# Performance work log

Hardware: AMD Instinct MI355X
Metric: run time of the kernel (lower is better)

## Reference

```python
import jax, jax.numpy as jnp
import numpy as np
from jax import lax

EPS = 1e-5

def _conv(x, w, pad):
    return lax.conv_general_dilated(x, w, (1, 1), [(pad, pad), (pad, pad)],
                                    dimension_numbers=('NCHW', 'OIHW', 'NCHW'))

def _bn(x, g, b, m, v):
    inv = g * jax.lax.rsqrt(v + EPS)
    return x * inv[None, :, None, None] + (b - m * inv)[None, :, None, None]

def _deform(x, ow, ob):
    # ConvOffset2d: 3x3 conv predicts 2*C per-channel (dy,dx) offsets, then
    # bilinear resample each channel at (grid + offset), clipped to the image.
    B, C, H, W = x.shape
    off = _conv(x, ow, 1) + ob[None, :, None, None]          # [B,2C,H,W]
    off = off.reshape(B, C, 2, H, W)
    yy = jnp.arange(H, dtype=x.dtype)[:, None]
    xx = jnp.arange(W, dtype=x.dtype)[None, :]
    py = jnp.clip(yy + off[:, :, 0], 0.0, H - 1)             # [B,C,H,W]
    px = jnp.clip(xx + off[:, :, 1], 0.0, W - 1)
    y0 = jnp.floor(py).astype(jnp.int32)
    x0 = jnp.floor(px).astype(jnp.int32)
    y1 = jnp.minimum(y0 + 1, H - 1)
    x1 = jnp.minimum(x0 + 1, W - 1)
    wy = py - y0.astype(x.dtype)
    wx = px - x0.astype(x.dtype)
    flat = x.reshape(B, C, H * W)
    def g(yi, xi):
        idx = (yi * W + xi).reshape(B, C, H * W)
        return jnp.take_along_axis(flat, idx, axis=2).reshape(B, C, H, W)
    v00, v01, v10, v11 = g(y0, x0), g(y0, x1), g(y1, x0), g(y1, x1)
    return (v00 * (1 - wy) * (1 - wx) + v01 * (1 - wy) * wx +
            v10 * wy * (1 - wx) + v11 * wy * wx)

def setup_inputs() -> dict:
    key = jax.random.key(0)
    ks = jax.random.split(key, 32)
    B, Cin, Cmid, H, W = 4, 1024, 256, 64, 64
    d = {}
    d['x'] = jax.random.normal(ks[0], (B, Cin, H, W), jnp.float32)
    # offset-predicting convs (3x3, C -> 2C), small init so offsets ~O(1)
    d['ow1'] = jax.random.normal(ks[1], (2 * Cin, Cin, 3, 3), jnp.float32) * 0.01
    d['ob1'] = jnp.zeros((2 * Cin,), jnp.float32)
    d['ow2'] = jax.random.normal(ks[2], (2 * Cmid, Cmid, 3, 3), jnp.float32) * 0.01
    d['ob2'] = jnp.zeros((2 * Cmid,), jnp.float32)
    d['ow3'] = jax.random.normal(ks[3], (2 * Cmid, Cmid, 3, 3), jnp.float32) * 0.01
    d['ob3'] = jnp.zeros((2 * Cmid,), jnp.float32)
    # bottleneck convs (no bias, as in ResNet)
    d['w1'] = jax.random.normal(ks[4], (Cmid, Cin, 1, 1), jnp.float32) * (1.0 / np.sqrt(Cin))
    d['w2'] = jax.random.normal(ks[5], (Cmid, Cmid, 3, 3), jnp.float32) * (1.0 / np.sqrt(9 * Cmid))
    d['w3'] = jax.random.normal(ks[6], (Cin, Cmid, 1, 1), jnp.float32) * (1.0 / np.sqrt(Cmid))
    # batchnorm (inference) params
    for i, c in zip((1, 2, 3), (Cmid, Cmid, Cin)):
        d[f'g{i}'] = jnp.ones((c,), jnp.float32)
        d[f'b{i}'] = jnp.zeros((c,), jnp.float32)
        d[f'm{i}'] = jax.random.normal(ks[10 + i], (c,), jnp.float32) * 0.1
        d[f'v{i}'] = jnp.ones((c,), jnp.float32) + jax.random.uniform(ks[20 + i], (c,), jnp.float32) * 0.1
    return d

def reference(x, ow1, ob1, w1, g1, b1, m1, v1,
              ow2, ob2, w2, g2, b2, m2, v2,
              ow3, ob3, w3, g3, b3, m3, v3):
    h = _deform(x, ow1, ob1)
    h = _bn(_conv(h, w1, 0), g1, b1, m1, v1)
    h = _deform(h, ow2, ob2)
    h = _bn(_conv(h, w2, 1), g2, b2, m2, v2)
    h = _deform(h, ow3, ob3)
    h = _bn(_conv(h, w3, 0), g3, b3, m3, v3)
    return jax.nn.relu(h)
```

## Files before the change

kernel.cpp:

```cpp
#include <hip/hip_runtime.h>


typedef unsigned short u16;
typedef __bf16 bf16x8 __attribute__((ext_vector_type(8)));
typedef float f32x4 __attribute__((ext_vector_type(4)));
typedef _Float16 f16;

__device__ __forceinline__ u16 f2bf(float f) {
  unsigned u = __float_as_uint(f);
  u += 0x7fffu + ((u >> 16) & 1u);
  return (u16)(u >> 16);
}
__device__ __forceinline__ float bf2f(u16 h) { return __uint_as_float((unsigned)h << 16); }
__device__ __forceinline__ u16 f2h(float f) { f16 h = (f16)f; return __builtin_bit_cast(u16, h); }
__device__ __forceinline__ float h2f(u16 u) { return (float)__builtin_bit_cast(f16, u); }

__device__ __forceinline__ void gload16(const u16* g, u16* l) {
  __builtin_amdgcn_global_load_lds((__attribute__((address_space(1))) unsigned int*)g,
                                   (__attribute__((address_space(3))) unsigned int*)l,
                                   16, 0, 0);
}

#define VM8() asm volatile("s_waitcnt vmcnt(8)" ::: "memory")
#define VM4() asm volatile("s_waitcnt vmcnt(4)" ::: "memory")
#define VM0() asm volatile("s_waitcnt vmcnt(0)" ::: "memory")
#define BAR()                                   \
  do {                                          \
    asm volatile("" ::: "memory");              \
    __builtin_amdgcn_s_barrier();               \
    asm volatile("" ::: "memory");              \
  } while (0)
#define LGK0()                                          \
  do {                                                  \
    asm volatile("s_waitcnt lgkmcnt(0)" ::: "memory");  \
    __builtin_amdgcn_sched_barrier(0);                  \
  } while (0)

__global__ __launch_bounds__(256) void zero_k(uint4* __restrict__ p, unsigned n) {
  unsigned i = blockIdx.x * 256u + threadIdx.x;
  const unsigned st = gridDim.x * 256u;
  uint4 z; z.x = 0u; z.y = 0u; z.z = 0u; z.w = 0u;
  for (; i < n; i += st) p[i] = z;
}

template <int SPLIT>
__global__ __launch_bounds__(256) void pack_w(const float* __restrict__ w,
                                              u16* __restrict__ hi, u16* __restrict__ lo,
                                              int M, int C, int T) {
  const int AK = C * T;
  const int id = blockIdx.x * 256 + threadIdx.x;
  if (id >= M * AK) return;
  const int j = id & 7;
  const int slot = (id >> 3) & 511;
  const int rest = id >> 12;
  const int steps = AK >> 5;
  const int step = rest % steps;
  const int mt = rest / steps;
  const int kg = slot >> 7, m = slot & 127;
  const int k = step * 32 + kg * 8 + j;
  const int tap = k / C;
  const int c = k - tap * C;
  const int mg = mt * 128 + m;
  const float v = w[((size_t)mg * C + c) * T + tap];
  const u16 h = f2bf(v);
  hi[id] = h;
  if (SPLIT) lo[id] = f2bf(v - bf2f(h));
}

template <int CC, int T>
__global__ __launch_bounds__(256) void pack8_w(const float* __restrict__ w,
                                               u16* __restrict__ dst, int M) {
  constexpr int KT2 = 2 * (T * CC / 64);
  const int id = blockIdx.x * 256 + threadIdx.x;
  if (id >= M * CC * T) return;
  const int j = id & 7;
  const int d = (id >> 3) & 1023;
  const int rest = id >> 13;
  const int H = rest % KT2;
  const int mt = rest / KT2;
  const int row = d >> 2, kq = d & 3;
  const int k = H * 32 + ((kq ^ ((row >> 1) & 3)) * 8) + j;
  const int tap = k / CC, c = k - tap * CC;
  const int oc = mt * 256 + row;
  dst[id] = f2bf(w[((size_t)oc * CC + c) * T + tap]);
}

__global__ __launch_bounds__(256) void prep_x(const float* __restrict__ x,
                                              u16* __restrict__ xp) {
  __shared__ float t[64][65];
  const int c0 = blockIdx.x * 64;
  const int y = blockIdx.y;
  const int b = blockIdx.z;
  const int tid = threadIdx.x;
#pragma unroll
  for (int i = 0; i < 16; ++i) {
    const int idx = i * 256 + tid;
    const int ci = idx >> 6, xi = idx & 63;
    t[ci][xi] = x[(((size_t)b * 1024 + c0 + ci) * 64 + y) * 64 + xi];
  }
  __syncthreads();
#pragma unroll
  for (int i = 0; i < 16; ++i) {
    const int idx = i * 256 + tid;
    const int xi = idx >> 6, ci = idx & 63;
    xp[((size_t)((b * 66 + y + 1) * 66 + (xi + 1))) * 1024 + c0 + ci] = f2bf(t[ci][xi]);
  }
}

template <int C, int PADDST>
__global__ __launch_bounds__(256) void deform_k(const u16* __restrict__ src,
                                                const u16* __restrict__ off,
                                                u16* __restrict__ dst) {
  const int id = blockIdx.x * 256 + threadIdx.x;
  const int c = id & (C - 1);
  const int pix = id / C;
  const int b = pix >> 12;
  const int y = (pix >> 6) & 63;
  const int x = pix & 63;
  const unsigned ov = *(const unsigned*)(off + (size_t)pix * (2 * C) + 2 * c);
  const float py = fminf(fmaxf((float)y + h2f((u16)(ov & 0xffffu)), 0.f), 63.f);
  const float px = fminf(fmaxf((float)x + h2f((u16)(ov >> 16)), 0.f), 63.f);
  const int y0i = (int)py, x0i = (int)px;
  const int y1i = min(y0i + 1, 63), x1i = min(x0i + 1, 63);
  const float wy = py - (float)y0i, wx = px - (float)x0i;
  const int bb66 = b * 66;
  auto at = [&](int yi, int xi) -> size_t {
    return ((size_t)((bb66 + yi + 1) * 66 + (xi + 1))) * C + c;
  };
  const float v00 = bf2f(src[at(y0i, x0i)]);
  const float v01 = bf2f(src[at(y0i, x1i)]);
  const float v10 = bf2f(src[at(y1i, x0i)]);
  const float v11 = bf2f(src[at(y1i, x1i)]);
  const float val = v00 * (1.f - wy) * (1.f - wx) + v01 * (1.f - wy) * wx +
                    v10 * wy * (1.f - wx) + v11 * wy * wx;
  const size_t d = PADDST ? at(y, x) : (size_t)id;
  dst[d] = f2bf(val);
}

template <int TAPS, int CC, int NMT>
__global__ __launch_bounds__(512, 2) void gemm8_conv(
    const u16* __restrict__ Apack, const u16* __restrict__ Bsrc,
    const float* __restrict__ bias, u16* __restrict__ out, int M) {
  constexpr int KT = TAPS * CC / 64;
  constexpr int KT2 = 2 * KT;
  __shared__ u16 lds[65536];
  const int tid = threadIdx.x;
  const int w = tid >> 6, lane = tid & 63;
  const int wm = w >> 2, wn = w & 3;
  const int kg = lane >> 4, lm = lane & 15;
  const int g = blockIdx.x;
  const int local = g >> 3;
  const int mt = local % NMT;
  const int nt = (g & 7) * 8 + local / NMT;
  const int b_img = nt >> 4;
  const int y0 = (nt & 15) * 4;
  const u16* Abase = Apack + (size_t)mt * KT2 * 8192;

  f32x4 acc[8][4];
  const f32x4 fz = {0.f, 0.f, 0.f, 0.f};
#pragma unroll
  for (int i = 0; i < 8; ++i)
#pragma unroll
    for (int j = 0; j < 4; ++j) acc[i][j] = fz;

  auto rbase = [&](int b, int op, int kh) -> unsigned {
    return (unsigned)(((b * 2 + op) * 2 + kh) * 8192);
  };
  auto stage = [&](int H, int op) {
    if (H >= KT2) return;
    const unsigned dstb = rbase((H >> 1) & 1, op, H & 1);
#pragma unroll
    for (int it = 0; it < 2; ++it) {
      const int d = it * 512 + tid;
      u16* ldst = (u16*)&lds[dstb + (unsigned)(it * 512 + (tid & ~63)) * 8];
      if (op == 0) {
        gload16(Abase + (size_t)H * 8192 + (size_t)d * 8, ldst);
      } else {
        const int pl = d >> 2, kq = d & 3;
        const int kglob = H * 32;
        const int tap = (TAPS == 1) ? 0 : (kglob / CC);
        const int cbase = kglob - tap * CC;
        const int ky = (TAPS == 9) ? tap / 3 : 0, kx = (TAPS == 9) ? tap % 3 : 0;
        const int r = pl >> 6, xc = pl & 63;
        const size_t gb = ((size_t)((b_img * 66 + y0 + r + ky) * 66 + (xc + kx))) * CC +
                          (size_t)(cbase + ((kq ^ ((pl >> 1) & 3)) * 8));
        gload16(Bsrc + gb, ldst);
      }
    }
  };

#define PHASE(MG_, KH_, STH_, STOP_, WAIT_)                                          \
  {                                                                                  \
    const unsigned regA = rbase(bi, 0, KH_);                                         \
    if (MG_ == 0) {                                                                  \
      const unsigned regB = rbase(bi, 1, KH_);                                       \
      _Pragma("unroll") for (int nf = 0; nf < 4; ++nf) {                             \
        const int pc = wn * 64 + nf * 16 + lm;                                       \
        bfrag[nf] = *(const bf16x8*)&lds[regB + pc * 32 + (kg ^ ((pc >> 1) & 3)) * 8]; \
      }                                                                              \
    }                                                                                \
    bf16x8 afrag[4];                                                                 \
    _Pragma("unroll") for (int f = 0; f < 4; ++f) {                                  \
      const int row = wm * 128 + (MG_ * 4 + f) * 16 + lm;                            \
      afrag[f] = *(const bf16x8*)&lds[regA + row * 32 + (kg ^ ((row >> 1) & 3)) * 8];  \
    }                                                                                \
    stage(STH_, STOP_);                                                              \
    BAR();                                                                           \
    LGK0();                                                                          \
    __builtin_amdgcn_s_setprio(1);                                                   \
    _Pragma("unroll") for (int f = 0; f < 4; ++f)                                    \
        _Pragma("unroll") for (int nf = 0; nf < 4; ++nf)                             \
            acc[MG_ * 4 + f][nf] = __builtin_amdgcn_mfma_f32_16x16x32_bf16(          \
                afrag[f], bfrag[nf], acc[MG_ * 4 + f][nf], 0, 0, 0);                 \
    __builtin_amdgcn_s_setprio(0);                                                   \
    WAIT_;                                                                           \
    BAR();                                                                           \
  }

  stage(0, 0); stage(0, 1);
  stage(1, 0); stage(1, 1);
  stage(2, 0); stage(2, 1);
  VM8();
  BAR();

  for (int t = 0; t < KT; ++t) {
    const int bi = t & 1;
    bf16x8 bfrag[4];
    PHASE(0, 0, 2 * t + 3, 0, (void)0);
    PHASE(1, 0, 2 * t + 3, 1, do { if (t == KT - 1) VM0(); else VM8(); } while (0));
    PHASE(0, 1, 2 * t + 4, 0, (void)0);
    PHASE(1, 1, 2 * t + 4, 1,
          do { if (t == KT - 2) VM4(); else if (t < KT - 2) VM8(); } while (0));
  }
#undef PHASE

  const int ocb = mt * 256 + wm * 128 + kg * 4;
#pragma unroll
  for (int mf = 0; mf < 8; ++mf) {
    const int oc0 = ocb + mf * 16;
    const f32x4 bv = *(const f32x4*)&bias[oc0];
#pragma unroll
    for (int nf = 0; nf < 4; ++nf) {
      const int pix = nt * 256 + wn * 64 + nf * 16 + lm;
      f32x4 r = acc[mf][nf] + bv;
      uint2 hv;
      hv.x = (unsigned)f2h(r[0]) | ((unsigned)f2h(r[1]) << 16);
      hv.y = (unsigned)f2h(r[2]) | ((unsigned)f2h(r[3]) << 16);
      *(uint2*)(out + (size_t)pix * M + oc0) = hv;
    }
  }
}

template <int TAPS, int PAD, int EPI, int CC, int WSPLIT>
__global__ __launch_bounds__(256, 2) void gemm_conv(
    const u16* __restrict__ Aph, const u16* __restrict__ Apl,
    const u16* __restrict__ Bh,
    const float* __restrict__ p0, const float* __restrict__ p1,
    const float* __restrict__ p2, const float* __restrict__ p3,
    float* __restrict__ outF, u16* __restrict__ o16a, int M) {
  constexpr int NB = 2 + WSPLIT;
  __shared__ u16 lds[NB * 4096];
  constexpr int steps = TAPS * (CC / 32);
  const int tid = threadIdx.x;
  const int w = tid >> 6, lane = tid & 63;
  const int wm = (w >> 1) * 64, wn = (w & 1) * 64;
  const int kg = lane >> 4, lm = lane & 15;
  const int wg = blockIdx.x;
  const int chunk = (int)(gridDim.x >> 3);
  const int g = (wg & 7) * chunk + (wg >> 3);
  const int mt = g >> 7, nt = g & 127;
  const int b_img = nt >> 5;
  const int y0 = (nt & 31) * 2;

  f32x4 acc[4][4];
  const f32x4 fz = {0.f, 0.f, 0.f, 0.f};
#pragma unroll
  for (int i = 0; i < 4; ++i)
#pragma unroll
    for (int j = 0; j < 4; ++j) acc[i][j] = fz;

  const u16* Abase_h = Aph + (size_t)mt * steps * 4096;
  const u16* Abase_l = WSPLIT ? (Apl + (size_t)mt * steps * 4096) : nullptr;

  for (int step = 0; step < steps; ++step) {
    const int tap = (TAPS == 1) ? 0 : (step / (CC / 32));
    const int c0 = (step - tap * (CC / 32)) * 32;
    const int ky = (TAPS == 9) ? (tap / 3) : 0;
    const int kx = (TAPS == 9) ? (tap % 3) : 0;

#pragma unroll
    for (int it = 0; it < 2; ++it) {
      const int slot = w * 128 + it * 64 + lane;
      const unsigned ldso = (unsigned)(w * 128 + it * 64) * 8u;
      const size_t ga = (size_t)step * 4096 + (size_t)slot * 8;
      gload16(Abase_h + ga, &lds[0 * 4096 + ldso]);
      if (WSPLIT) gload16(Abase_l + ga, &lds[1 * 4096 + ldso]);
      const int n = slot >> 2, kq = slot & 3;
      const int kga = kq ^ ((n >> 1) & 3);
      size_t gb;
      if (PAD) {
        const int r = n >> 6, xc = n & 63;
        gb = ((size_t)((b_img * 66 + (y0 + r + ky)) * 66 + (xc + kx))) * CC +
             (size_t)(c0 + kga * 8);
      } else {
        gb = (size_t)(nt * 128 + n) * CC + (size_t)(c0 + kga * 8);
      }
      gload16(Bh + gb, &lds[(NB - 1) * 4096 + ldso]);
    }
    __syncthreads();

    bf16x8 ah[4], al[4], bh[4];
#pragma unroll
    for (int f = 0; f < 4; ++f) {
      const unsigned ao = (unsigned)(kg * 128 + wm + f * 16 + lm) * 8u;
      ah[f] = *(const bf16x8*)&lds[0 * 4096 + ao];
      if (WSPLIT) al[f] = *(const bf16x8*)&lds[1 * 4096 + ao];
      const int n = wn + f * 16 + lm;
      const unsigned bo = (unsigned)(n * 4 + (kg ^ ((n >> 1) & 3))) * 8u;
      bh[f] = *(const bf16x8*)&lds[(NB - 1) * 4096 + bo];
    }
#pragma unroll
    for (int i = 0; i < 4; ++i)
#pragma unroll
      for (int j = 0; j < 4; ++j) {
        acc[i][j] = __builtin_amdgcn_mfma_f32_16x16x32_bf16(ah[i], bh[j], acc[i][j], 0, 0, 0);
        if (WSPLIT)
          acc[i][j] = __builtin_amdgcn_mfma_f32_16x16x32_bf16(al[i], bh[j], acc[i][j], 0, 0, 0);
      }
    __syncthreads();
  }

  const int ocb = mt * 128 + wm + kg * 4;
#pragma unroll
  for (int fi = 0; fi < 4; ++fi) {
    const int oc0 = ocb + fi * 16;
    f32x4 scl, sft;
    if (EPI == 0) {
#pragma unroll
      for (int j = 0; j < 4; ++j) { scl[j] = 1.f; sft[j] = p0[oc0 + j]; }
    } else {
#pragma unroll
      for (int j = 0; j < 4; ++j) {
        const float inv = p0[oc0 + j] / sqrtf(p3[oc0 + j] + 1e-5f);
        scl[j] = inv;
        sft[j] = p1[oc0 + j] - p2[oc0 + j] * inv;
      }
    }
#pragma unroll
    for (int fj = 0; fj < 4; ++fj) {
      const int pix = nt * 128 + wn + fj * 16 + lm;
      f32x4 r = acc[fi][fj] * scl + sft;
      if (EPI == 0) {
        uint2 hv;
        hv.x = (unsigned)f2h(r[0]) | ((unsigned)f2h(r[1]) << 16);
        hv.y = (unsigned)f2h(r[2]) | ((unsigned)f2h(r[3]) << 16);
        *(uint2*)(o16a + (size_t)pix * M + oc0) = hv;
      } else if (EPI == 1) {
        const int bb = pix >> 12, yy = (pix >> 6) & 63, xx = pix & 63;
        const size_t pp = ((size_t)((bb * 66 + yy + 1) * 66 + (xx + 1))) * M + oc0;
        uint2 hv;
        hv.x = (unsigned)f2bf(r[0]) | ((unsigned)f2bf(r[1]) << 16);
        hv.y = (unsigned)f2bf(r[2]) | ((unsigned)f2bf(r[3]) << 16);
        *(uint2*)(o16a + pp) = hv;
      } else {
        const int bb = pix >> 12, pin = pix & 4095;
#pragma unroll
        for (int j = 0; j < 4; ++j)
          outF[((size_t)(bb * M + oc0 + j)) * 4096 + pin] = fmaxf(r[j], 0.f);
      }
    }
  }
}

extern "C" void kernel_launch(void* const* d_in, const int* in_sizes, int n_in,
                              void* d_out, int out_size, void* d_ws, size_t ws_size,
                              hipStream_t stream) {
  (void)in_sizes; (void)out_size;
  if (n_in < 22) return;
  const float* x   = (const float*)d_in[0];
  const float* ow1 = (const float*)d_in[1];
  const float* ob1 = (const float*)d_in[2];
  const float* ow2 = (const float*)d_in[3];
  const float* ob2 = (const float*)d_in[4];
  const float* ow3 = (const float*)d_in[5];
  const float* ob3 = (const float*)d_in[6];
  const float* w1  = (const float*)d_in[7];
  const float* w2  = (const float*)d_in[8];
  const float* w3  = (const float*)d_in[9];
  const float* g1 = (const float*)d_in[10], *b1 = (const float*)d_in[11];
  const float* m1 = (const float*)d_in[12], *v1 = (const float*)d_in[13];
  const float* g2 = (const float*)d_in[14], *b2 = (const float*)d_in[15];
  const float* m2 = (const float*)d_in[16], *v2 = (const float*)d_in[17];
  const float* g3 = (const float*)d_in[18], *b3 = (const float*)d_in[19];
  const float* m3 = (const float*)d_in[20], *v3 = (const float*)d_in[21];

  char* W = (char*)d_ws;
  constexpr size_t P66_1024 = 4ull * 66 * 66 * 1024 * 2;
  constexpr size_t P66_256  = 4ull * 66 * 66 * 256 * 2;
  constexpr size_t SZ_OFF1  = 4ull * 4096 * 2048 * 2;
  constexpr size_t SZ_OFF2  = 4ull * 4096 * 512 * 2;
  constexpr size_t SZ_H1    = 4ull * 4096 * 1024 * 2;
  constexpr size_t SZ_H3    = 4ull * 4096 * 256 * 2;
  constexpr size_t SZ_OW1 = 2048ull * 9216 * 2;
  constexpr size_t SZ_W1  = 256ull * 1024 * 2;
  constexpr size_t SZ_OW2 = 512ull * 2304 * 2;
  constexpr size_t SZ_W2  = 256ull * 2304 * 2;
  constexpr size_t SZ_OW3 = 512ull * 2304 * 2;
  constexpr size_t SZ_W3  = 1024ull * 256 * 2;

  constexpr size_t o_ow1h = 0;
  constexpr size_t o_xp   = o_ow1h + SZ_OW1;
  constexpr size_t o_off1 = o_xp + P66_1024;
  constexpr size_t o_t1p  = o_off1;
  constexpr size_t o_off2 = o_t1p + P66_256;
  constexpr size_t o_h2p  = o_off2 + SZ_OFF2;
  constexpr size_t o_t2p  = o_h2p + P66_256;
  static_assert(o_t2p + P66_256 <= o_off1 + SZ_OFF1, "era2 fits off1 slot");
  constexpr size_t o_h1   = o_off1 + SZ_OFF1;
  constexpr size_t o_off3 = o_h1;
  constexpr size_t o_h3   = o_off3 + SZ_OFF2;
  static_assert(o_h3 + SZ_H3 <= o_h1 + SZ_H1, "off3+h3 fit h1 slot");
  constexpr size_t o_w1h  = o_h1 + SZ_H1;
  constexpr size_t o_w1l  = o_w1h + SZ_W1;
  constexpr size_t o_ow2h = o_w1l + SZ_W1;
  constexpr size_t o_w2h  = o_ow2h + SZ_OW2;
  constexpr size_t o_w2l  = o_w2h + SZ_W2;
  constexpr size_t o_ow3h = o_w2l + SZ_W2;
  constexpr size_t o_w3h  = o_ow3h + SZ_OW3;
  constexpr size_t o_w3l  = o_w3h + SZ_W3;
  constexpr size_t WS_NEED = o_w3l + SZ_W3;
  if (ws_size < WS_NEED) return;

  auto U = [&](size_t o) { return (u16*)(W + o); };
  auto zero = [&](size_t off, size_t bytes) {
    const unsigned n = (unsigned)(bytes / 16);
    unsigned grid = (n + 255) / 256; if (grid > 4096) grid = 4096;
    zero_k<<<grid, 256, 0, stream>>>((uint4*)(W + off), n);
  };

  {
    int n;
    n = 2048 * 9216; pack8_w<1024, 9><<<(n + 255) / 256, 256, 0, stream>>>(ow1, U(o_ow1h), 2048);
    n = 512 * 2304;  pack8_w<256, 9><<<(n + 255) / 256, 256, 0, stream>>>(ow2, U(o_ow2h), 512);
    n = 512 * 2304;  pack8_w<256, 9><<<(n + 255) / 256, 256, 0, stream>>>(ow3, U(o_ow3h), 512);
    n = 256 * 1024;  pack_w<1><<<(n + 255) / 256, 256, 0, stream>>>(w1, U(o_w1h), U(o_w1l), 256, 1024, 1);
    n = 256 * 2304;  pack_w<1><<<(n + 255) / 256, 256, 0, stream>>>(w2, U(o_w2h), U(o_w2l), 256, 256, 9);
    n = 1024 * 256;  pack_w<1><<<(n + 255) / 256, 256, 0, stream>>>(w3, U(o_w3h), U(o_w3l), 1024, 256, 1);
  }

  zero(o_xp, P66_1024);
  prep_x<<<dim3(16, 64, 4), 256, 0, stream>>>(x, U(o_xp));

  gemm8_conv<9, 1024, 8><<<512, 512, 0, stream>>>(
      U(o_ow1h), U(o_xp), ob1, U(o_off1), 2048);
  deform_k<1024, 0><<<65536, 256, 0, stream>>>(U(o_xp), U(o_off1), U(o_h1));

  zero(o_t1p, P66_256);
  zero(o_h2p, 2 * P66_256);
  gemm_conv<1, 0, 1, 1024, 1><<<256, 256, 0, stream>>>(
      U(o_w1h), U(o_w1l), U(o_h1), g1, b1, m1, v1, nullptr, U(o_t1p), 256);
  gemm8_conv<9, 256, 2><<<128, 512, 0, stream>>>(
      U(o_ow2h), U(o_t1p), ob2, U(o_off2), 512);
  deform_k<256, 1><<<16384, 256, 0, stream>>>(U(o_t1p), U(o_off2), U(o_h2p));
  gemm_conv<9, 1, 1, 256, 1><<<256, 256, 0, stream>>>(
      U(o_w2h), U(o_w2l), U(o_h2p), g2, b2, m2, v2, nullptr, U(o_t2p), 256);
  gemm8_conv<9, 256, 2><<<128, 512, 0, stream>>>(
      U(o_ow3h), U(o_t2p), ob3, U(o_off3), 512);
  deform_k<256, 0><<<16384, 256, 0, stream>>>(U(o_t2p), U(o_off3), U(o_h3));
  gemm_conv<1, 0, 2, 256, 1><<<1024, 256, 0, stream>>>(
      U(o_w3h), U(o_w3l), U(o_h3), g3, b3, m3, v3, (float*)d_out, nullptr, 1024);
}
```

Before: 1.128 ms.

## Software-pipeline LDS fragment reads in gemm8 and drop split-bf16 weight precision

Restructures the big offset-conv GEMM main loop so LDS fragment reads for the next MFMA group are issued before the current group's MFMAs, with per-lane global addresses precomputed once and A/B staging split into separate issue points. Separately switches all bottleneck and small offset convs from hi/lo split-bf16 weights to single bf16 (SPLIT=0), removing the lo workspace and halving MFMA work there. The small offset convs also move from gemm8_conv to gemm_conv. Precision drop risks accuracy, and the reordered waitcnt schedule risks hazards.

```diff
diff --git a/kernel.cpp b/kernel.cpp
--- a/kernel.cpp
+++ b/kernel.cpp
@@ -22,7 +22,7 @@
 }
 
 #define VM8() asm volatile("s_waitcnt vmcnt(8)" ::: "memory")
-#define VM4() asm volatile("s_waitcnt vmcnt(4)" ::: "memory")
+#define VM6() asm volatile("s_waitcnt vmcnt(6)" ::: "memory")
 #define VM0() asm volatile("s_waitcnt vmcnt(0)" ::: "memory")
 #define BAR()                                   \
   do {                                          \
@@ -35,6 +35,7 @@
     asm volatile("s_waitcnt lgkmcnt(0)" ::: "memory");  \
     __builtin_amdgcn_sched_barrier(0);                  \
   } while (0)
+#define SB0() __builtin_amdgcn_sched_barrier(0)
 
 __global__ __launch_bounds__(256) void zero_k(uint4* __restrict__ p, unsigned n) {
   unsigned i = blockIdx.x * 256u + threadIdx.x;
@@ -154,7 +155,20 @@
   const int nt = (g & 7) * 8 + local / NMT;
   const int b_img = nt >> 4;
   const int y0 = (nt & 15) * 4;
+
+  int laneA[2], laneB[2];
+  unsigned ldsoff[2];
+#pragma unroll
+  for (int it = 0; it < 2; ++it) {
+    const int d = it * 512 + tid;
+    laneA[it] = d * 8;
+    const int pl = d >> 2, kq = d & 3;
+    const int r = pl >> 6, xc = pl & 63;
+    laneB[it] = (r * 66 + xc) * CC + (kq ^ ((pl >> 1) & 3)) * 8;
+    ldsoff[it] = (unsigned)(it * 512 + (tid & ~63)) * 8u;
+  }
   const u16* Abase = Apack + (size_t)mt * KT2 * 8192;
+  const u16* Bbase = Bsrc + (size_t)(b_img * 66 + y0) * 66 * CC;
 
   f32x4 acc[8][4];
   const f32x4 fz = {0.f, 0.f, 0.f, 0.f};
@@ -166,73 +180,95 @@
   auto rbase = [&](int b, int op, int kh) -> unsigned {
     return (unsigned)(((b * 2 + op) * 2 + kh) * 8192);
   };
-  auto stage = [&](int H, int op) {
+  auto stageA = [&](int H) {
     if (H >= KT2) return;
-    const unsigned dstb = rbase((H >> 1) & 1, op, H & 1);
-#pragma unroll
-    for (int it = 0; it < 2; ++it) {
-      const int d = it * 512 + tid;
-      u16* ldst = (u16*)&lds[dstb + (unsigned)(it * 512 + (tid & ~63)) * 8];
-      if (op == 0) {
-        gload16(Abase + (size_t)H * 8192 + (size_t)d * 8, ldst);
-      } else {
-        const int pl = d >> 2, kq = d & 3;
-        const int kglob = H * 32;
-        const int tap = (TAPS == 1) ? 0 : (kglob / CC);
-        const int cbase = kglob - tap * CC;
-        const int ky = (TAPS == 9) ? tap / 3 : 0, kx = (TAPS == 9) ? tap % 3 : 0;
-        const int r = pl >> 6, xc = pl & 63;
-        const size_t gb = ((size_t)((b_img * 66 + y0 + r + ky) * 66 + (xc + kx))) * CC +
-                          (size_t)(cbase + ((kq ^ ((pl >> 1) & 3)) * 8));
-        gload16(Bsrc + gb, ldst);
-      }
-    }
-  };
-
-#define PHASE(MG_, KH_, STH_, STOP_, WAIT_)                                          \
-  {                                                                                  \
-    const unsigned regA = rbase(bi, 0, KH_);                                         \
-    if (MG_ == 0) {                                                                  \
-      const unsigned regB = rbase(bi, 1, KH_);                                       \
-      _Pragma("unroll") for (int nf = 0; nf < 4; ++nf) {                             \
-        const int pc = wn * 64 + nf * 16 + lm;                                       \
-        bfrag[nf] = *(const bf16x8*)&lds[regB + pc * 32 + (kg ^ ((pc >> 1) & 3)) * 8]; \
-      }                                                                              \
-    }                                                                                \
-    bf16x8 afrag[4];                                                                 \
-    _Pragma("unroll") for (int f = 0; f < 4; ++f) {                                  \
-      const int row = wm * 128 + (MG_ * 4 + f) * 16 + lm;                            \
-      afrag[f] = *(const bf16x8*)&lds[regA + row * 32 + (kg ^ ((row >> 1) & 3)) * 8];  \
-    }                                                                                \
-    stage(STH_, STOP_);                                                              \
-    BAR();                                                                           \
-    LGK0();                                                                          \
+    const u16* p = Abase + (size_t)H * 8192;
+    const unsigned db = rbase((H >> 1) & 1, 0, H & 1);
+    gload16(p + laneA[0], (u16*)&lds[db + ldsoff[0]]);
+    gload16(p + laneA[1], (u16*)&lds[db + ldsoff[1]]);
+  };
+  auto stageB = [&](int H) {
+    if (H >= KT2) return;
+    const int kglob = H * 32;
+    const int tap = (TAPS == 1) ? 0 : (kglob / CC);
+    const int cbase = kglob - tap * CC;
+    const int ky = (TAPS == 9) ? tap / 3 : 0, kx = (TAPS == 9) ? tap % 3 : 0;
+    const u16* p = Bbase + (ky * 66 + kx) * CC + cbase;
+    const unsigned db = rbase((H >> 1) & 1, 1, H & 1);
+    gload16(p + laneB[0], (u16*)&lds[db + ldsoff[0]]);
+    gload16(p + laneB[1], (u16*)&lds[db + ldsoff[1]]);
+  };
+
+  bf16x8 afE[4], afO[4], bfA[4], bfB[4];
+  auto rdA = [&](bf16x8* dst, int buf, int kh, int MG) {
+    const unsigned regA = rbase(buf, 0, kh);
+#pragma unroll
+    for (int f = 0; f < 4; ++f) {
+      const int row = wm * 128 + (MG * 4 + f) * 16 + lm;
+      dst[f] = *(const bf16x8*)&lds[regA + row * 32 + (kg ^ ((row >> 1) & 3)) * 8];
+    }
+  };
+  auto rdB = [&](bf16x8* dst, int buf, int kh) {
+    const unsigned regB = rbase(buf, 1, kh);
+#pragma unroll
+    for (int f = 0; f < 4; ++f) {
+      const int pc = wn * 64 + f * 16 + lm;
+      dst[f] = *(const bf16x8*)&lds[regB + pc * 32 + (kg ^ ((pc >> 1) & 3)) * 8];
+    }
+  };
+
+#define MFMA16(MG_, AF_, BF_)                                                        \
+  do {                                                                               \
     __builtin_amdgcn_s_setprio(1);                                                   \
     _Pragma("unroll") for (int f = 0; f < 4; ++f)                                    \
         _Pragma("unroll") for (int nf = 0; nf < 4; ++nf)                             \
             acc[MG_ * 4 + f][nf] = __builtin_amdgcn_mfma_f32_16x16x32_bf16(          \
-                afrag[f], bfrag[nf], acc[MG_ * 4 + f][nf], 0, 0, 0);                 \
+                AF_[f], BF_[nf], acc[MG_ * 4 + f][nf], 0, 0, 0);                     \
     __builtin_amdgcn_s_setprio(0);                                                   \
-    WAIT_;                                                                           \
-    BAR();                                                                           \
-  }
-
-  stage(0, 0); stage(0, 1);
-  stage(1, 0); stage(1, 1);
-  stage(2, 0); stage(2, 1);
+  } while (0)
+
+  stageA(0); stageB(0);
+  stageA(1); stageB(1);
+  stageA(2); stageB(2);
   VM8();
   BAR();
+  rdA(afE, 0, 0, 0);
+  rdB(bfA, 0, 0);
 
   for (int t = 0; t < KT; ++t) {
     const int bi = t & 1;
-    bf16x8 bfrag[4];
-    PHASE(0, 0, 2 * t + 3, 0, (void)0);
-    PHASE(1, 0, 2 * t + 3, 1, do { if (t == KT - 1) VM0(); else VM8(); } while (0));
-    PHASE(0, 1, 2 * t + 4, 0, (void)0);
-    PHASE(1, 1, 2 * t + 4, 1,
-          do { if (t == KT - 2) VM4(); else if (t < KT - 2) VM8(); } while (0));
-  }
-#undef PHASE
+    LGK0();
+    rdA(afO, bi, 0, 1);
+    stageA(2 * t + 3);
+    SB0();
+    MFMA16(0, afE, bfA);
+    if (t >= KT - 2) VM0(); else VM6();
+    BAR();
+    LGK0();
+    rdA(afE, bi, 1, 0);
+    rdB(bfB, bi, 1);
+    stageB(2 * t + 3);
+    SB0();
+    MFMA16(1, afO, bfA);
+    BAR();
+    LGK0();
+    rdA(afO, bi, 1, 1);
+    stageA(2 * t + 4);
+    SB0();
+    MFMA16(0, afE, bfB);
+    if (t < KT - 2) VM6();
+    BAR();
+    LGK0();
+    if (t + 1 < KT) {
+      rdA(afE, bi ^ 1, 0, 0);
+      rdB(bfA, bi ^ 1, 0);
+    }
+    stageB(2 * t + 4);
+    SB0();
+    MFMA16(1, afO, bfB);
+    BAR();
+  }
+#undef MFMA16
 
   const int ocb = mt * 256 + wm * 128 + kg * 4;
 #pragma unroll
@@ -421,14 +457,11 @@
   constexpr size_t o_h3   = o_off3 + SZ_OFF2;
   static_assert(o_h3 + SZ_H3 <= o_h1 + SZ_H1, "off3+h3 fit h1 slot");
   constexpr size_t o_w1h  = o_h1 + SZ_H1;
-  constexpr size_t o_w1l  = o_w1h + SZ_W1;
-  constexpr size_t o_ow2h = o_w1l + SZ_W1;
+  constexpr size_t o_ow2h = o_w1h + SZ_W1;
   constexpr size_t o_w2h  = o_ow2h + SZ_OW2;
-  constexpr size_t o_w2l  = o_w2h + SZ_W2;
-  constexpr size_t o_ow3h = o_w2l + SZ_W2;
+  constexpr size_t o_ow3h = o_w2h + SZ_W2;
   constexpr size_t o_w3h  = o_ow3h + SZ_OW3;
-  constexpr size_t o_w3l  = o_w3h + SZ_W3;
-  constexpr size_t WS_NEED = o_w3l + SZ_W3;
+  constexpr size_t WS_NEED = o_w3h + SZ_W3;
   if (ws_size < WS_NEED) return;
 
   auto U = [&](size_t o) { return (u16*)(W + o); };
@@ -441,11 +474,11 @@
   {
     int n;
     n = 2048 * 9216; pack8_w<1024, 9><<<(n + 255) / 256, 256, 0, stream>>>(ow1, U(o_ow1h), 2048);
-    n = 512 * 2304;  pack8_w<256, 9><<<(n + 255) / 256, 256, 0, stream>>>(ow2, U(o_ow2h), 512);
-    n = 512 * 2304;  pack8_w<256, 9><<<(n + 255) / 256, 256, 0, stream>>>(ow3, U(o_ow3h), 512);
-    n = 256 * 1024;  pack_w<1><<<(n + 255) / 256, 256, 0, stream>>>(w1, U(o_w1h), U(o_w1l), 256, 1024, 1);
-    n = 256 * 2304;  pack_w<1><<<(n + 255) / 256, 256, 0, stream>>>(w2, U(o_w2h), U(o_w2l), 256, 256, 9);
-    n = 1024 * 256;  pack_w<1><<<(n + 255) / 256, 256, 0, stream>>>(w3, U(o_w3h), U(o_w3l), 1024, 256, 1);
+    n = 512 * 2304;  pack_w<0><<<(n + 255) / 256, 256, 0, stream>>>(ow2, U(o_ow2h), nullptr, 512, 256, 9);
+    n = 512 * 2304;  pack_w<0><<<(n + 255) / 256, 256, 0, stream>>>(ow3, U(o_ow3h), nullptr, 512, 256, 9);
+    n = 256 * 1024;  pack_w<0><<<(n + 255) / 256, 256, 0, stream>>>(w1, U(o_w1h), nullptr, 256, 1024, 1);
+    n = 256 * 2304;  pack_w<0><<<(n + 255) / 256, 256, 0, stream>>>(w2, U(o_w2h), nullptr, 256, 256, 9);
+    n = 1024 * 256;  pack_w<0><<<(n + 255) / 256, 256, 0, stream>>>(w3, U(o_w3h), nullptr, 1024, 256, 1);
   }
 
   zero(o_xp, P66_1024);
@@ -457,16 +490,18 @@
 
   zero(o_t1p, P66_256);
   zero(o_h2p, 2 * P66_256);
-  gemm_conv<1, 0, 1, 1024, 1><<<256, 256, 0, stream>>>(
-      U(o_w1h), U(o_w1l), U(o_h1), g1, b1, m1, v1, nullptr, U(o_t1p), 256);
-  gemm8_conv<9, 256, 2><<<128, 512, 0, stream>>>(
-      U(o_ow2h), U(o_t1p), ob2, U(o_off2), 512);
+  gemm_conv<1, 0, 1, 1024, 0><<<256, 256, 0, stream>>>(
+      U(o_w1h), nullptr, U(o_h1), g1, b1, m1, v1, nullptr, U(o_t1p), 256);
+  gemm_conv<9, 1, 0, 256, 0><<<512, 256, 0, stream>>>(
+      U(o_ow2h), nullptr, U(o_t1p), ob2, nullptr, nullptr, nullptr,
+      nullptr, U(o_off2), 512);
   deform_k<256, 1><<<16384, 256, 0, stream>>>(U(o_t1p), U(o_off2), U(o_h2p));
-  gemm_conv<9, 1, 1, 256, 1><<<256, 256, 0, stream>>>(
-      U(o_w2h), U(o_w2l), U(o_h2p), g2, b2, m2, v2, nullptr, U(o_t2p), 256);
-  gemm8_conv<9, 256, 2><<<128, 512, 0, stream>>>(
-      U(o_ow3h), U(o_t2p), ob3, U(o_off3), 512);
+  gemm_conv<9, 1, 1, 256, 0><<<256, 256, 0, stream>>>(
+      U(o_w2h), nullptr, U(o_h2p), g2, b2, m2, v2, nullptr, U(o_t2p), 256);
+  gemm_conv<9, 1, 0, 256, 0><<<512, 256, 0, stream>>>(
+      U(o_ow3h), nullptr, U(o_t2p), ob3, nullptr, nullptr, nullptr,
+      nullptr, U(o_off3), 512);
   deform_k<256, 0><<<16384, 256, 0, stream>>>(U(o_t2p), U(o_off3), U(o_h3));
-  gemm_conv<1, 0, 2, 256, 1><<<1024, 256, 0, stream>>>(
-      U(o_w3h), U(o_w3l), U(o_h3), g3, b3, m3, v3, (float*)d_out, nullptr, 1024);
-}
+  gemm_conv<1, 0, 2, 256, 0><<<1024, 256, 0, stream>>>(
+      U(o_w3h), nullptr, U(o_h3), g3, b3, m3, v3, (float*)d_out, nullptr, 1024);
+}
```

Measured after the change: 1.056 ms. 6.4% less time.
